# Kernel tuning notes

Hardware: AMD Instinct MI355X
Metric: run time of the kernel (lower is better)

The kernel has to match this reference:

```python
import jax, jax.numpy as jnp
import numpy as np

ALPHA = 0.5
MODES = 12288  # == C*H*W, required by view_as in the original module
WIDTH = 512
B, C, H, W = 256, 3, 64, 64


def _linear_params(key, fan_in, fan_out):
    # torch.nn.Linear default init: U(-1/sqrt(fan_in), 1/sqrt(fan_in))
    k1, k2 = jax.random.split(key)
    s = 1.0 / np.sqrt(fan_in)
    Wm = jax.random.uniform(k1, (fan_in, fan_out), jnp.float32, -s, s)
    b = jax.random.uniform(k2, (fan_out,), jnp.float32, -s, s)
    return Wm, b


def setup_inputs() -> dict:
    key = jax.random.key(0)
    ks = jax.random.split(key, 6)
    x = jax.random.normal(ks[0], (B, C, H, W), jnp.float32)
    Ws1, bs1 = _linear_params(ks[1], MODES, WIDTH)   # spectral_operator
    Ws2, bs2 = _linear_params(ks[2], WIDTH, MODES)
    Wn1, bn1 = _linear_params(ks[3], MODES, WIDTH)   # neural_operator
    Wn2, bn2 = _linear_params(ks[4], WIDTH, WIDTH)
    Wn3, bn3 = _linear_params(ks[5], WIDTH, MODES)
    return {"x": x, "Ws1": Ws1, "bs1": bs1, "Ws2": Ws2, "bs2": bs2,
            "Wn1": Wn1, "bn1": bn1, "Wn2": Wn2, "bn2": bn2, "Wn3": Wn3, "bn3": bn3}


def _gl_fractional(f, alpha):
    """Grunwald-Letnikov fractional derivative on a 1-D signal sampled on
    t = linspace(0, 1, N):  D^a f[k] = h^{-a} * sum_{j<=k} w_j f[k-j],
    w_0 = 1, w_j = w_{j-1} * (j-1-a)/j  (i.e. (-1)^j * binom(a, j)).
    Implemented as an O(N log N) causal FFT convolution."""
    N = f.shape[0]
    j = jnp.arange(1, N, dtype=jnp.float32)
    w = jnp.concatenate([jnp.ones((1,), jnp.float32), jnp.cumprod((j - 1.0 - alpha) / j)])
    L = 2 * N  # >= N + N - 1 -> linear (causal) convolution
    conv = jnp.fft.irfft(jnp.fft.rfft(f, L) * jnp.fft.rfft(w, L), L)[:N]
    h = 1.0 / (N - 1)
    return conv * np.float32(h ** (-alpha))


def reference(x, Ws1, bs1, Ws2, bs2, Wn1, bn1, Wn2, bn2, Wn3, bn3):
    b, c, hh, ww = x.shape
    # (dead-code encoder branch of the original is omitted: its output x_frac
    #  is never used downstream)
    x_freq = jnp.fft.fft2(x, axes=(-2, -1))                 # complex64 (B,C,H,W)
    # _apply_fractional_operator: flattens the WHOLE real part into one signal
    fr = _gl_fractional(jnp.real(x_freq).reshape(-1), ALPHA).reshape(b, -1)  # (B, MODES)
    # spectral_operator: Linear -> ReLU -> Linear  (modes == C*H*W so [:modes] is identity)
    spec = jax.nn.relu(fr @ Ws1 + bs1) @ Ws2 + bs2          # (B, MODES)
    # neural_operator: Linear -> ReLU -> Linear -> ReLU -> Linear
    h1 = jax.nn.relu(spec @ Wn1 + bn1)
    h2 = jax.nn.relu(h1 @ Wn2 + bn2)
    proc = (h2 @ Wn3 + bn3).reshape(b, c, hh, ww)
    # complex(proc, 0) -> ifft2 -> real
    return jnp.real(jnp.fft.ifft2(proc.astype(jnp.complex64), axes=(-2, -1)))
```

## Files before the change

### kernel.cpp

```cpp
#include <hip/hip_runtime.h>
#include <hip/hip_bf16.h>

#define NTOT 3145728
#define NIMG 768
#define CTAPS 1024
#define NBAND 66

typedef __attribute__((ext_vector_type(8)))  short bf16x8;
typedef __attribute__((ext_vector_type(4)))  short bf16x4;
typedef __attribute__((ext_vector_type(8)))  unsigned short u16x8;
typedef __attribute__((ext_vector_type(4)))  unsigned short u16x4;
typedef __attribute__((ext_vector_type(4)))  unsigned uint32x4;
typedef __attribute__((ext_vector_type(4)))  float f32x4;
typedef __attribute__((ext_vector_type(16))) float f32x16;

__device__ inline unsigned short f2bf(float x) {
    unsigned u = __builtin_bit_cast(unsigned, x);
    u += 0x7fffu + ((u >> 16) & 1u);
    return (unsigned short)(u >> 16);
}
__device__ inline float bf2f(unsigned short u) {
    return __builtin_bit_cast(float, (unsigned)u << 16);
}
__device__ inline void split2(float v, unsigned short& hi, unsigned short& lo) {
    hi = f2bf(v);
    lo = f2bf(v - bf2f(hi));
}
__device__ inline unsigned cvt_pk_bf16(float a, float b) {
    unsigned r;
    asm("v_cvt_pk_bf16_f32 %0, %1, %2" : "=v"(r) : "v"(a), "v"(b));
    return r;
}
__device__ inline bf16x8 ld2(const unsigned short* p) {
    bf16x4 a = *(const bf16x4*)p;
    bf16x4 b = *(const bf16x4*)(p + 4);
    bf16x8 r;
    #pragma unroll
    for (int i = 0; i < 4; ++i) { r[i] = a[i]; r[4 + i] = b[i]; }
    return r;
}

__global__ __launch_bounds__(1024)
void gen_tables(unsigned short* __restrict__ Tch, unsigned short* __restrict__ Tsh,
                unsigned short* __restrict__ Bth,
                unsigned short* __restrict__ fph, unsigned short* __restrict__ fpl)
{
    __shared__ float wsm[CTAPS];
    const int tid = threadIdx.x;
    const int bid = blockIdx.x;
    const float step = 6.28318530717958647692f / 64.0f;
    if (tid < 512) {
        int i = bid * 512 + tid;
        int p = i >> 6, q = i & 63;
        float ang = (float)((p * q) & 63) * step;
        Tch[i] = f2bf(cosf(ang));
        Tsh[i] = f2bf(sinf(ang));
    }
    if (bid == 0) { fph[tid] = 0; fpl[tid] = 0; }
    if (tid < 64) {
        const int l = tid;
        float vals[16];
        float local = 1.0f;
        #pragma unroll
        for (int m = 0; m < 16; ++m) {
            int j = 16 * l + 1 + m;
            local *= ((float)j - 1.5f) / (float)j;
            vals[m] = local;
        }
        float scan = local;
        #pragma unroll
        for (int d = 1; d < 64; d <<= 1) {
            float o = __shfl_up(scan, (unsigned)d, 64);
            if (l >= d) scan *= o;
        }
        float prefix = __shfl_up(scan, 1u, 64);
        if (l == 0) prefix = 1.0f;
        const float s = sqrtf((float)(NTOT - 1));
        if (l == 0) wsm[0] = s;
        #pragma unroll
        for (int m = 0; m < 16; ++m) {
            int j = 16 * l + 1 + m;
            if (j < CTAPS) wsm[j] = prefix * vals[m] * s;
        }
    }
    __syncthreads();
    const int i0 = bid * 4224;
    for (int i = i0 + tid; i < i0 + 4224; i += 1024) {
        int d = (i >> 9) - 1, o = (i >> 4) & 31, u = i & 15;
        int j = 16 * d + o - u;
        Bth[i] = (j >= 0 && j < CTAPS) ? f2bf(wsm[j]) : (unsigned short)0;
    }
}

template<int INV>
__global__ __launch_bounds__(256)
void dft_mfma(const void* __restrict__ Xin, const unsigned short* __restrict__ Xlo_in,
              const unsigned short* __restrict__ Tch, const unsigned short* __restrict__ Tsh,
              void* __restrict__ Out, unsigned short* __restrict__ Out2)
{
    __shared__ __align__(16) unsigned short Xh[64 * 68], Xl[64 * 68];
    __shared__ __align__(16) unsigned short Chh[64 * 68], Cll[64 * 68];
    __shared__ __align__(16) unsigned short Shh[64 * 68], Sll[64 * 68];
    const int tid = threadIdx.x;
    const int img = blockIdx.x;
    {
        const int rr = tid >> 2, c0 = (tid & 3) * 16;
        const int lb = rr * 68 + c0;
        if (!INV) {
            const float* Xf = (const float*)Xin + (size_t)img * 4096 + rr * 64 + c0;
            #pragma unroll
            for (int i = 0; i < 4; ++i) {
                float4 v = *(const float4*)(Xf + 4 * i);
                float vv[4] = {v.x, v.y, v.z, v.w};
                #pragma unroll
                for (int k = 0; k < 4; ++k) {
                    unsigned short h, l; split2(vv[k], h, l);
                    Xh[lb + 4 * i + k] = h; Xl[lb + 4 * i + k] = l;
                }
            }
        } else {
            const unsigned short* Ph = (const unsigned short*)Xin + (size_t)img * 4096 + rr * 64 + c0;
            const unsigned short* Pl = Xlo_in + (size_t)img * 4096 + rr * 64 + c0;
            #pragma unroll
            for (int i = 0; i < 4; ++i) {
                *(ushort4*)&Xh[lb + 4 * i] = *(const ushort4*)(Ph + 4 * i);
                *(ushort4*)&Xl[lb + 4 * i] = *(const ushort4*)(Pl + 4 * i);
            }
        }
    }
    __syncthreads();

    const int lane = tid & 63, wv = tid >> 6;
    const int r = lane & 31, g = lane >> 5;
    const int q0 = (wv >> 1) * 32, r0 = (wv & 1) * 32;
    const int tA = (q0 + r) * 64;
    const int xB = (r0 + r) * 68;

    f32x16 a1, a2;
    #pragma unroll
    for (int i = 0; i < 16; ++i) { a1[i] = 0.f; a2[i] = 0.f; }
    #pragma unroll
    for (int ks = 0; ks < 4; ++ks) {
        const int ko = ks * 16 + 8 * g;
        bf16x8 xh = ld2(&Xh[xB + ko]);
        bf16x8 xl = ld2(&Xl[xB + ko]);
        bf16x8 th = *(const bf16x8*)&Tch[tA + ko];
        a1 = __builtin_amdgcn_mfma_f32_32x32x16_bf16(th, xh, a1, 0, 0, 0);
        a2 = __builtin_amdgcn_mfma_f32_32x32x16_bf16(th, xl, a2, 0, 0, 0);
    }
    #pragma unroll
    for (int reg = 0; reg < 16; ++reg) {
        int qq = q0 + (reg & 3) + 8 * (reg >> 2) + 4 * g;
        unsigned short h, l; split2(a1[reg] + a2[reg], h, l);
        Chh[qq * 68 + r0 + r] = h; Cll[qq * 68 + r0 + r] = l;
    }
    #pragma unroll
    for (int i = 0; i < 16; ++i) { a1[i] = 0.f; a2[i] = 0.f; }
    #pragma unroll
    for (int ks = 0; ks < 4; ++ks) {
        const int ko = ks * 16 + 8 * g;
        bf16x8 xh = ld2(&Xh[xB + ko]);
        bf16x8 xl = ld2(&Xl[xB + ko]);
        bf16x8 th = *(const bf16x8*)&Tsh[tA + ko];
        a1 = __builtin_amdgcn_mfma_f32_32x32x16_bf16(th, xh, a1, 0, 0, 0);
        a2 = __builtin_amdgcn_mfma_f32_32x32x16_bf16(th, xl, a2, 0, 0, 0);
    }
    #pragma unroll
    for (int reg = 0; reg < 16; ++reg) {
        int qq = q0 + (reg & 3) + 8 * (reg >> 2) + 4 * g;
        unsigned short h, l; split2(-(a1[reg] + a2[reg]), h, l);
        Shh[qq * 68 + r0 + r] = h; Sll[qq * 68 + r0 + r] = l;
    }
    __syncthreads();

    #pragma unroll
    for (int i = 0; i < 16; ++i) { a1[i] = 0.f; a2[i] = 0.f; }
    #pragma unroll
    for (int ks = 0; ks < 4; ++ks) {
        const int ko = ks * 16 + 8 * g;
        bf16x8 ch = ld2(&Chh[xB + ko]);
        bf16x8 cl = ld2(&Cll[xB + ko]);
        bf16x8 th = *(const bf16x8*)&Tch[tA + ko];
        a1 = __builtin_amdgcn_mfma_f32_32x32x16_bf16(th, ch, a1, 0, 0, 0);
        a2 = __builtin_amdgcn_mfma_f32_32x32x16_bf16(th, cl, a2, 0, 0, 0);
        bf16x8 sh = ld2(&Shh[xB + ko]);
        bf16x8 sl = ld2(&Sll[xB + ko]);
        bf16x8 uh = *(const bf16x8*)&Tsh[tA + ko];
        a1 = __builtin_amdgcn_mfma_f32_32x32x16_bf16(uh, sh, a1, 0, 0, 0);
        a2 = __builtin_amdgcn_mfma_f32_32x32x16_bf16(uh, sl, a2, 0, 0, 0);
    }
    #pragma unroll
    for (int reg = 0; reg < 16; ++reg) {
        int pp = q0 + (reg & 3) + 8 * (reg >> 2) + 4 * g;
        float v = a1[reg] + a2[reg];
        size_t oi = (size_t)img * 4096 + (size_t)pp * 64 + r0 + r;
        if (INV) {
            ((float*)Out)[oi] = v * (1.0f / 4096.0f);
        } else {
            unsigned short h, l; split2(v, h, l);
            ((unsigned short*)Out)[oi] = h; Out2[oi] = l;
        }
    }
}

__global__ __launch_bounds__(256)
void conv_mfma(const unsigned short* __restrict__ fh, const unsigned short* __restrict__ fl,
               const unsigned short* __restrict__ Bth,
               unsigned short* __restrict__ fr)
{
    __shared__ __align__(16) unsigned short Ah[5120], Al[5120];
    const int tid = threadIdx.x;
    const size_t tb0 = (size_t)blockIdx.x * 4096;
    {
        const unsigned short* sh = fh + tb0 - 1024;
        const unsigned short* sl = fl + tb0 - 1024;
        for (int gg = tid; gg < 640; gg += 256) {
            int off = (gg ^ ((gg >> 3) & 7)) << 3;
            *(bf16x8*)&Ah[off] = *(const bf16x8*)(sh + gg * 8);
            *(bf16x8*)&Al[off] = *(const bf16x8*)(sl + gg * 8);
        }
    }
    __syncthreads();

    const int lane = tid & 63;
    const int wv = tid >> 6;
    const int r = lane & 31, g = lane >> 5;
    const int bo = 16 * r + 8 * g;
    const int base_gg = 128 * (wv + 1) + 4 * r + g + 2;

    f32x16 a1, a2;
    #pragma unroll
    for (int i = 0; i < 16; ++i) { a1[i] = 0.f; a2[i] = 0.f; }

    const unsigned short* bhp = Bth + bo;
    bf16x8 bh0 = *(const bf16x8*)(bhp);
    bf16x8 bh1 = *(const bf16x8*)(bhp + 512);

    for (int dd = 0; dd < NBAND; dd += 2) {
        bf16x8 nh0, nh1;
        if (dd + 2 < NBAND) {
            nh0 = *(const bf16x8*)(bhp + 512 * (dd + 2));
            nh1 = *(const bf16x8*)(bhp + 512 * (dd + 3));
        }
        {
            int gg = base_gg - 2 * dd;
            int off = (gg ^ ((gg >> 3) & 7)) << 3;
            bf16x8 avh = *(const bf16x8*)&Ah[off];
            bf16x8 avl = *(const bf16x8*)&Al[off];
            a1 = __builtin_amdgcn_mfma_f32_32x32x16_bf16(avh, bh0, a1, 0, 0, 0);
            a2 = __builtin_amdgcn_mfma_f32_32x32x16_bf16(avl, bh0, a2, 0, 0, 0);
        }
        {
            int gg = base_gg - 2 * (dd + 1);
            int off = (gg ^ ((gg >> 3) & 7)) << 3;
            bf16x8 avh = *(const bf16x8*)&Ah[off];
            bf16x8 avl = *(const bf16x8*)&Al[off];
            a1 = __builtin_amdgcn_mfma_f32_32x32x16_bf16(avh, bh1, a1, 0, 0, 0);
            a2 = __builtin_amdgcn_mfma_f32_32x32x16_bf16(avl, bh1, a2, 0, 0, 0);
        }
        bh0 = nh0; bh1 = nh1;
    }

    const size_t tb = tb0 + 1024 * wv;
    #pragma unroll
    for (int reg = 0; reg < 16; ++reg) {
        int row = (reg & 3) + 8 * (reg >> 2) + 4 * g;
        fr[tb + 32 * row + r] = f2bf(a1[reg] + a2[reg]);
    }
}

template<int MODE, int RELU>
__global__ __launch_bounds__(256)
void gemm_nb(const unsigned short* __restrict__ A, const float* __restrict__ W,
             void* __restrict__ Out, const float* __restrict__ bias,
             int M, int N, int K, int kChunk, int nbn,
             unsigned short* __restrict__ Out2)
{
    const int tid = threadIdx.x;
    const int id = blockIdx.x;
    const int gq = id >> 4, rr = id & 15;
    const int t  = gq * 8 + (rr & 7);
    const int bm = (rr >> 3) * 128;
    const int bn = (t % nbn) * 64;
    const int z  = t / nbn;
    const int kb0 = z * kChunk;
    const int nsteps = kChunk >> 5;

    const int lane = tid & 63, wv = tid >> 6;
    const int wr = (wv >> 1) * 64, wc = (wv & 1) * 32;
    const int l15 = lane & 15, l4 = lane >> 4;

    f32x4 acc[4][2];
    #pragma unroll
    for (int i = 0; i < 4; ++i)
        #pragma unroll
        for (int j = 0; j < 2; ++j)
            acc[i][j] = (f32x4){0.f, 0.f, 0.f, 0.f};

    const unsigned short* Arow = A + (size_t)(bm + wr + l15) * K + l4 * 8;
    const float* Wcol = W + bn + wc + l15;

    bf16x8 fa0[4], fa1[4];
    float fw0[16], fw1[16];

#define LOADA(F, kb) { _Pragma("unroll") for (int m4 = 0; m4 < 4; ++m4)                   \
    F[m4] = *(const bf16x8*)(Arow + (kb) + (size_t)m4 * 16 * K); }
#define LOADW(R, kb) { const float* p_ = Wcol + (size_t)((kb) + l4 * 8) * N;              \
    _Pragma("unroll") for (int e = 0; e < 8; ++e) {                                       \
        R[e] = p_[(size_t)e * N]; R[8 + e] = p_[(size_t)e * N + 16]; } }
#define CVTW(Fb, R) {                                                                     \
    uint32x4 v0_, v1_;                                                                    \
    _Pragma("unroll") for (int e = 0; e < 4; ++e) {                                       \
        v0_[e] = cvt_pk_bf16(R[2 * e], R[2 * e + 1]);                                     \
        v1_[e] = cvt_pk_bf16(R[8 + 2 * e], R[8 + 2 * e + 1]); }                           \
    Fb[0] = __builtin_bit_cast(bf16x8, v0_);                                              \
    Fb[1] = __builtin_bit_cast(bf16x8, v1_); }
#define MFMA_CL(fa_, fb_) { _Pragma("unroll") for (int m4 = 0; m4 < 4; ++m4)              \
    _Pragma("unroll") for (int n4 = 0; n4 < 2; ++n4)                                      \
        acc[m4][n4] = __builtin_amdgcn_mfma_f32_16x16x32_bf16(fa_[m4], fb_[n4], acc[m4][n4], 0, 0, 0); }

    LOADA(fa0, kb0);      LOADW(fw0, kb0);
    LOADA(fa1, kb0 + 32); LOADW(fw1, kb0 + 32);

    for (int s = 0; s < nsteps; s += 2) {
        {
            bf16x8 ac[4], bc[2];
            #pragma unroll
            for (int m4 = 0; m4 < 4; ++m4) ac[m4] = fa0[m4];
            CVTW(bc, fw0);
            if (s + 2 < nsteps) { LOADA(fa0, kb0 + (s + 2) * 32); LOADW(fw0, kb0 + (s + 2) * 32); }
            MFMA_CL(ac, bc);
        }
        {
            bf16x8 ac[4], bc[2];
            #pragma unroll
            for (int m4 = 0; m4 < 4; ++m4) ac[m4] = fa1[m4];
            CVTW(bc, fw1);
            if (s + 3 < nsteps) { LOADA(fa1, kb0 + (s + 3) * 32); LOADW(fw1, kb0 + (s + 3) * 32); }
            MFMA_CL(ac, bc);
        }
    }
#undef LOADA
#undef LOADW
#undef CVTW
#undef MFMA_CL

    #pragma unroll
    for (int m4 = 0; m4 < 4; ++m4)
        #pragma unroll
        for (int n4 = 0; n4 < 2; ++n4) {
            const int col = bn + wc + n4 * 16 + l15;
            const int row0 = bm + wr + m4 * 16 + l4 * 4;
            #pragma unroll
            for (int rg = 0; rg < 4; ++rg) {
                float v = acc[m4][n4][rg];
                const size_t oi = (size_t)(row0 + rg) * N + col;
                if (MODE == 0) {
                    ((float*)Out)[(size_t)z * M * N + oi] = v;
                } else {
                    v += bias[col];
                    if (RELU) v = fmaxf(v, 0.f);
                    if (MODE == 1) {
                        ((float*)Out)[oi] = v;
                    } else if (MODE == 2) {
                        ((unsigned short*)Out)[oi] = f2bf(v);
                    } else {
                        unsigned short h, l; split2(v, h, l);
                        ((unsigned short*)Out)[oi] = h; Out2[oi] = l;
                    }
                }
            }
        }
}

template<int RELU, int OUTBF>
__global__ __launch_bounds__(256)
void reduce_bias(const float* __restrict__ P, const float* __restrict__ bias,
                 void* __restrict__ C, int MN, int N, int S)
{
    const int idx4 = blockIdx.x * 256 + threadIdx.x;
    const int MN4 = MN >> 2;
    if (idx4 >= MN4) return;
    const float4* P4 = (const float4*)P;
    float4 a = P4[idx4];
    for (int zz = 1; zz < S; ++zz) {
        float4 b = P4[(size_t)zz * MN4 + idx4];
        a.x += b.x; a.y += b.y; a.z += b.z; a.w += b.w;
    }
    int n0 = (idx4 * 4) % N;
    a.x += bias[n0]; a.y += bias[n0 + 1]; a.z += bias[n0 + 2]; a.w += bias[n0 + 3];
    if (RELU) {
        a.x = fmaxf(a.x, 0.f); a.y = fmaxf(a.y, 0.f);
        a.z = fmaxf(a.z, 0.f); a.w = fmaxf(a.w, 0.f);
    }
    if (OUTBF) {
        ushort4 v = {f2bf(a.x), f2bf(a.y), f2bf(a.z), f2bf(a.w)};
        ((ushort4*)C)[idx4] = v;
    } else {
        ((float4*)C)[idx4] = a;
    }
}

extern "C" void kernel_launch(void* const* d_in, const int* in_sizes, int n_in,
                              void* d_out, int out_size, void* d_ws, size_t ws_size,
                              hipStream_t stream)
{
    const float* x   = (const float*)d_in[0];
    const float* Ws1 = (const float*)d_in[1];
    const float* bs1 = (const float*)d_in[2];
    const float* Ws2 = (const float*)d_in[3];
    const float* bs2 = (const float*)d_in[4];
    const float* Wn1 = (const float*)d_in[5];
    const float* bn1 = (const float*)d_in[6];
    const float* Wn2 = (const float*)d_in[7];
    const float* bn2 = (const float*)d_in[8];
    const float* Wn3 = (const float*)d_in[9];
    const float* bn3 = (const float*)d_in[10];
    float* out = (float*)d_out;

    char* p = (char*)d_ws;
    auto alloc = [&](size_t bytes) { char* q = p; p += (bytes + 255) & ~(size_t)255; return q; };
    unsigned short* Tch = (unsigned short*)alloc(8192);
    unsigned short* Tsh = (unsigned short*)alloc(8192);
    unsigned short* Bth = (unsigned short*)alloc((size_t)NBAND * 512 * 2);
    unsigned short* fhb = (unsigned short*)alloc((size_t)(1024 + NTOT) * 2);
    unsigned short* flb = (unsigned short*)alloc((size_t)(1024 + NTOT) * 2);
    unsigned short* fr   = (unsigned short*)alloc((size_t)NTOT * 2);
    unsigned short* spec = (unsigned short*)alloc((size_t)NTOT * 2);
    unsigned short* ph   = (unsigned short*)alloc((size_t)NTOT * 2);
    unsigned short* pl   = (unsigned short*)alloc((size_t)NTOT * 2);
    unsigned short* t1   = (unsigned short*)alloc(262144);
    unsigned short* h1   = (unsigned short*)alloc(262144);
    unsigned short* h2   = (unsigned short*)alloc(262144);
    float* part          = (float*)alloc((size_t)16 * 131072 * 4);

    gen_tables<<<8, 1024, 0, stream>>>(Tch, Tsh, Bth, fhb, flb);

    dft_mfma<0><<<NIMG, 256, 0, stream>>>(x, nullptr, Tch, Tsh,
                                          fhb + 1024, flb + 1024);

    conv_mfma<<<NTOT / 4096, 256, 0, stream>>>(fhb + 1024, flb + 1024, Bth, fr);

    gemm_nb<0, 0><<<256, 256, 0, stream>>>(fr, Ws1, part, nullptr,
                                           256, 512, 12288, 768, 8, nullptr);
    reduce_bias<1, 1><<<128, 256, 0, stream>>>(part, bs1, t1, 131072, 512, 16);
    gemm_nb<2, 0><<<384, 256, 0, stream>>>(t1, Ws2, spec, bs2,
                                           256, 12288, 512, 512, 192, nullptr);

    gemm_nb<0, 0><<<256, 256, 0, stream>>>(spec, Wn1, part, nullptr,
                                           256, 512, 12288, 768, 8, nullptr);
    reduce_bias<1, 1><<<128, 256, 0, stream>>>(part, bn1, h1, 131072, 512, 16);
    gemm_nb<0, 0><<<128, 256, 0, stream>>>(h1, Wn2, part, nullptr,
                                           256, 512, 512, 64, 8, nullptr);
    reduce_bias<1, 1><<<128, 256, 0, stream>>>(part, bn2, h2, 131072, 512, 8);
    gemm_nb<3, 0><<<384, 256, 0, stream>>>(h2, Wn3, ph, bn3,
                                           256, 12288, 512, 512, 192, pl);

    dft_mfma<1><<<NIMG, 256, 0, stream>>>(ph, pl, Tch, Tsh, out, nullptr);
}
```

Measured before the change: 148.9 us.

## Drop split-bf16 low part in inverse DFT and remap split-K GEMM blocks

The inverse DFT path now uses only the bf16 high part of the final projection instead of a hi/lo split pair. That halves its MFMAs, LDS traffic and intermediate stores, and the last GEMM no longer writes the low-part buffer. The split-K GEMMs also get a new block-index mapping (XMAP=1) that groups blocks sharing the same N tile across K chunks, to improve L2 reuse of weights. The cost is lower precision in the inverse transform, which may loosen accuracy against the reference.

Result: faster. 143.8 us (-3.5%).

```diff
diff --git a/kernel.cpp b/kernel.cpp
--- a/kernel.cpp
+++ b/kernel.cpp
@@ -94,19 +94,22 @@
 
 template<int INV>
 __global__ __launch_bounds__(256)
-void dft_mfma(const void* __restrict__ Xin, const unsigned short* __restrict__ Xlo_in,
+void dft_mfma(const void* __restrict__ Xin,
               const unsigned short* __restrict__ Tch, const unsigned short* __restrict__ Tsh,
               void* __restrict__ Out, unsigned short* __restrict__ Out2)
 {
-    __shared__ __align__(16) unsigned short Xh[64 * 68], Xl[64 * 68];
-    __shared__ __align__(16) unsigned short Chh[64 * 68], Cll[64 * 68];
-    __shared__ __align__(16) unsigned short Shh[64 * 68], Sll[64 * 68];
+    __shared__ __align__(16) unsigned short Xh[64 * 68];
+    __shared__ __align__(16) unsigned short Xl[INV ? 16 : 64 * 68];
+    __shared__ __align__(16) unsigned short Chh[64 * 68];
+    __shared__ __align__(16) unsigned short Cll[INV ? 16 : 64 * 68];
+    __shared__ __align__(16) unsigned short Shh[64 * 68];
+    __shared__ __align__(16) unsigned short Sll[INV ? 16 : 64 * 68];
     const int tid = threadIdx.x;
     const int img = blockIdx.x;
     {
         const int rr = tid >> 2, c0 = (tid & 3) * 16;
         const int lb = rr * 68 + c0;
-        if (!INV) {
+        if constexpr (!INV) {
             const float* Xf = (const float*)Xin + (size_t)img * 4096 + rr * 64 + c0;
             #pragma unroll
             for (int i = 0; i < 4; ++i) {
@@ -120,12 +123,9 @@
             }
         } else {
             const unsigned short* Ph = (const unsigned short*)Xin + (size_t)img * 4096 + rr * 64 + c0;
-            const unsigned short* Pl = Xlo_in + (size_t)img * 4096 + rr * 64 + c0;
             #pragma unroll
-            for (int i = 0; i < 4; ++i) {
+            for (int i = 0; i < 4; ++i)
                 *(ushort4*)&Xh[lb + 4 * i] = *(const ushort4*)(Ph + 4 * i);
-                *(ushort4*)&Xl[lb + 4 * i] = *(const ushort4*)(Pl + 4 * i);
-            }
         }
     }
     __syncthreads();
@@ -143,16 +143,22 @@
     for (int ks = 0; ks < 4; ++ks) {
         const int ko = ks * 16 + 8 * g;
         bf16x8 xh = ld2(&Xh[xB + ko]);
-        bf16x8 xl = ld2(&Xl[xB + ko]);
         bf16x8 th = *(const bf16x8*)&Tch[tA + ko];
         a1 = __builtin_amdgcn_mfma_f32_32x32x16_bf16(th, xh, a1, 0, 0, 0);
-        a2 = __builtin_amdgcn_mfma_f32_32x32x16_bf16(th, xl, a2, 0, 0, 0);
+        if constexpr (!INV) {
+            bf16x8 xl = ld2(&Xl[xB + ko]);
+            a2 = __builtin_amdgcn_mfma_f32_32x32x16_bf16(th, xl, a2, 0, 0, 0);
+        }
     }
     #pragma unroll
     for (int reg = 0; reg < 16; ++reg) {
         int qq = q0 + (reg & 3) + 8 * (reg >> 2) + 4 * g;
-        unsigned short h, l; split2(a1[reg] + a2[reg], h, l);
-        Chh[qq * 68 + r0 + r] = h; Cll[qq * 68 + r0 + r] = l;
+        if constexpr (!INV) {
+            unsigned short h, l; split2(a1[reg] + a2[reg], h, l);
+            Chh[qq * 68 + r0 + r] = h; Cll[qq * 68 + r0 + r] = l;
+        } else {
+            Chh[qq * 68 + r0 + r] = f2bf(a1[reg]);
+        }
     }
     #pragma unroll
     for (int i = 0; i < 16; ++i) { a1[i] = 0.f; a2[i] = 0.f; }
@@ -160,16 +166,22 @@
     for (int ks = 0; ks < 4; ++ks) {
         const int ko = ks * 16 + 8 * g;
         bf16x8 xh = ld2(&Xh[xB + ko]);
-        bf16x8 xl = ld2(&Xl[xB + ko]);
         bf16x8 th = *(const bf16x8*)&Tsh[tA + ko];
         a1 = __builtin_amdgcn_mfma_f32_32x32x16_bf16(th, xh, a1, 0, 0, 0);
-        a2 = __builtin_amdgcn_mfma_f32_32x32x16_bf16(th, xl, a2, 0, 0, 0);
+        if constexpr (!INV) {
+            bf16x8 xl = ld2(&Xl[xB + ko]);
+            a2 = __builtin_amdgcn_mfma_f32_32x32x16_bf16(th, xl, a2, 0, 0, 0);
+        }
     }
     #pragma unroll
     for (int reg = 0; reg < 16; ++reg) {
         int qq = q0 + (reg & 3) + 8 * (reg >> 2) + 4 * g;
-        unsigned short h, l; split2(-(a1[reg] + a2[reg]), h, l);
-        Shh[qq * 68 + r0 + r] = h; Sll[qq * 68 + r0 + r] = l;
+        if constexpr (!INV) {
+            unsigned short h, l; split2(-(a1[reg] + a2[reg]), h, l);
+            Shh[qq * 68 + r0 + r] = h; Sll[qq * 68 + r0 + r] = l;
+        } else {
+            Shh[qq * 68 + r0 + r] = f2bf(-a1[reg]);
+        }
     }
     __syncthreads();
 
@@ -179,25 +191,26 @@
     for (int ks = 0; ks < 4; ++ks) {
         const int ko = ks * 16 + 8 * g;
         bf16x8 ch = ld2(&Chh[xB + ko]);
-        bf16x8 cl = ld2(&Cll[xB + ko]);
         bf16x8 th = *(const bf16x8*)&Tch[tA + ko];
         a1 = __builtin_amdgcn_mfma_f32_32x32x16_bf16(th, ch, a1, 0, 0, 0);
-        a2 = __builtin_amdgcn_mfma_f32_32x32x16_bf16(th, cl, a2, 0, 0, 0);
         bf16x8 sh = ld2(&Shh[xB + ko]);
-        bf16x8 sl = ld2(&Sll[xB + ko]);
         bf16x8 uh = *(const bf16x8*)&Tsh[tA + ko];
         a1 = __builtin_amdgcn_mfma_f32_32x32x16_bf16(uh, sh, a1, 0, 0, 0);
-        a2 = __builtin_amdgcn_mfma_f32_32x32x16_bf16(uh, sl, a2, 0, 0, 0);
+        if constexpr (!INV) {
+            bf16x8 cl = ld2(&Cll[xB + ko]);
+            a2 = __builtin_amdgcn_mfma_f32_32x32x16_bf16(th, cl, a2, 0, 0, 0);
+            bf16x8 sl = ld2(&Sll[xB + ko]);
+            a2 = __builtin_amdgcn_mfma_f32_32x32x16_bf16(uh, sl, a2, 0, 0, 0);
+        }
     }
     #pragma unroll
     for (int reg = 0; reg < 16; ++reg) {
         int pp = q0 + (reg & 3) + 8 * (reg >> 2) + 4 * g;
-        float v = a1[reg] + a2[reg];
         size_t oi = (size_t)img * 4096 + (size_t)pp * 64 + r0 + r;
-        if (INV) {
-            ((float*)Out)[oi] = v * (1.0f / 4096.0f);
+        if constexpr (INV) {
+            ((float*)Out)[oi] = a1[reg] * (1.0f / 4096.0f);
         } else {
-            unsigned short h, l; split2(v, h, l);
+            unsigned short h, l; split2(a1[reg] + a2[reg], h, l);
             ((unsigned short*)Out)[oi] = h; Out2[oi] = l;
         }
     }
@@ -269,20 +282,29 @@
     }
 }
 
-template<int MODE, int RELU>
+template<int MODE, int RELU, int XMAP>
 __global__ __launch_bounds__(256)
 void gemm_nb(const unsigned short* __restrict__ A, const float* __restrict__ W,
              void* __restrict__ Out, const float* __restrict__ bias,
-             int M, int N, int K, int kChunk, int nbn,
+             int M, int N, int K, int kChunk, int nbn, int nz,
              unsigned short* __restrict__ Out2)
 {
     const int tid = threadIdx.x;
     const int id = blockIdx.x;
-    const int gq = id >> 4, rr = id & 15;
-    const int t  = gq * 8 + (rr & 7);
-    const int bm = (rr >> 3) * 128;
-    const int bn = (t % nbn) * 64;
-    const int z  = t / nbn;
+    int bm, bn, z;
+    if (XMAP == 0) {
+        const int gq = id >> 4, rr = id & 15;
+        const int t  = gq * 8 + (rr & 7);
+        bm = (rr >> 3) * 128;
+        bn = (t % nbn) * 64;
+        z  = t / nbn;
+    } else {
+        const int x = id & 7, j = id >> 3;
+        const int p = x + 8 * (j / nbn);
+        bn = (j % nbn) * 64;
+        bm = (p / nz) * 128;
+        z  = p % nz;
+    }
     const int kb0 = z * kChunk;
     const int nsteps = kChunk >> 5;
 
@@ -428,7 +450,6 @@
     unsigned short* fr   = (unsigned short*)alloc((size_t)NTOT * 2);
     unsigned short* spec = (unsigned short*)alloc((size_t)NTOT * 2);
     unsigned short* ph   = (unsigned short*)alloc((size_t)NTOT * 2);
-    unsigned short* pl   = (unsigned short*)alloc((size_t)NTOT * 2);
     unsigned short* t1   = (unsigned short*)alloc(262144);
     unsigned short* h1   = (unsigned short*)alloc(262144);
     unsigned short* h2   = (unsigned short*)alloc(262144);
@@ -436,25 +457,24 @@
 
     gen_tables<<<8, 1024, 0, stream>>>(Tch, Tsh, Bth, fhb, flb);
 
-    dft_mfma<0><<<NIMG, 256, 0, stream>>>(x, nullptr, Tch, Tsh,
-                                          fhb + 1024, flb + 1024);
+    dft_mfma<0><<<NIMG, 256, 0, stream>>>(x, Tch, Tsh, fhb + 1024, flb + 1024);
 
     conv_mfma<<<NTOT / 4096, 256, 0, stream>>>(fhb + 1024, flb + 1024, Bth, fr);
 
-    gemm_nb<0, 0><<<256, 256, 0, stream>>>(fr, Ws1, part, nullptr,
-                                           256, 512, 12288, 768, 8, nullptr);
+    gemm_nb<0, 0, 1><<<256, 256, 0, stream>>>(fr, Ws1, part, nullptr,
+                                              256, 512, 12288, 768, 8, 16, nullptr);
     reduce_bias<1, 1><<<128, 256, 0, stream>>>(part, bs1, t1, 131072, 512, 16);
-    gemm_nb<2, 0><<<384, 256, 0, stream>>>(t1, Ws2, spec, bs2,
-                                           256, 12288, 512, 512, 192, nullptr);
-
-    gemm_nb<0, 0><<<256, 256, 0, stream>>>(spec, Wn1, part, nullptr,
-                                           256, 512, 12288, 768, 8, nullptr);
+    gemm_nb<2, 0, 0><<<384, 256, 0, stream>>>(t1, Ws2, spec, bs2,
+                                              256, 12288, 512, 512, 192, 1, nullptr);
+
+    gemm_nb<0, 0, 1><<<256, 256, 0, stream>>>(spec, Wn1, part, nullptr,
+                                              256, 512, 12288, 768, 8, 16, nullptr);
     reduce_bias<1, 1><<<128, 256, 0, stream>>>(part, bn1, h1, 131072, 512, 16);
-    gemm_nb<0, 0><<<128, 256, 0, stream>>>(h1, Wn2, part, nullptr,
-                                           256, 512, 512, 64, 8, nullptr);
+    gemm_nb<0, 0, 1><<<128, 256, 0, stream>>>(h1, Wn2, part, nullptr,
+                                              256, 512, 512, 64, 8, 8, nullptr);
     reduce_bias<1, 1><<<128, 256, 0, stream>>>(part, bn2, h2, 131072, 512, 8);
-    gemm_nb<3, 0><<<384, 256, 0, stream>>>(h2, Wn3, ph, bn3,
-                                           256, 12288, 512, 512, 192, pl);
-
-    dft_mfma<1><<<NIMG, 256, 0, stream>>>(ph, pl, Tch, Tsh, out, nullptr);
-}
+    gemm_nb<2, 0, 0><<<384, 256, 0, stream>>>(h2, Wn3, ph, bn3,
+                                              256, 12288, 512, 512, 192, 1, nullptr);
+
+    dft_mfma<1><<<NIMG, 256, 0, stream>>>(ph, Tch, Tsh, out, nullptr);
+}
```
